# Performance work log

Measured on AMD Instinct MI355X. Metric: run time of the kernel, lower is better.

The kernel has to match this reference:

```python
import jax, jax.numpy as jnp
import numpy as np

B, S, DIN, DOUT, H = 4, 2048, 512, 512, 8
DH = DOUT // H
EPS = 1e-5


def _conv_bn(x, conv_w, conv_b, bn_gamma, bn_beta, bn_mean, bn_var):
    # x: [B, S, DIN] -> permute to [B, DIN, S] like torch
    xc = jnp.transpose(x, (0, 2, 1))
    y = jax.lax.conv_general_dilated(
        xc, conv_w, window_strides=(1,), padding=[(3, 3)],
        dimension_numbers=('NCH', 'OIH', 'NCH'))  # [B, DOUT, S]
    y = y + conv_b[None, :, None]
    # BatchNorm1d in eval mode: normalize per channel with running stats
    inv = jax.lax.rsqrt(bn_var + EPS)
    y = (y - bn_mean[None, :, None]) * (inv * bn_gamma)[None, :, None] + bn_beta[None, :, None]
    return jnp.transpose(y, (0, 2, 1))  # back to [B, S, DOUT]


def setup_inputs() -> dict:
    key = jax.random.key(0)
    ks = jax.random.split(key, 4)
    return {
        'q': jax.random.normal(ks[0], (B, S, DIN), dtype=jnp.float32),
        'k': jax.random.normal(ks[1], (B, S, DIN), dtype=jnp.float32),
        'v': jax.random.normal(ks[2], (B, S, DIN), dtype=jnp.float32),
        'conv_w': jax.random.normal(ks[3], (DOUT, DIN, 7), dtype=jnp.float32) * 0.02,
        'conv_b': jnp.zeros((DOUT,), jnp.float32),
        'bn_gamma': jnp.ones((DOUT,), jnp.float32),
        'bn_beta': jnp.zeros((DOUT,), jnp.float32),
        'bn_mean': jnp.zeros((DOUT,), jnp.float32),
        'bn_var': jnp.ones((DOUT,), jnp.float32),
        'ln_gamma': jnp.ones((DOUT,), jnp.float32),
        'ln_beta': jnp.zeros((DOUT,), jnp.float32),
    }


def reference(q, k, v, conv_w, conv_b, bn_gamma, bn_beta, bn_mean, bn_var,
              ln_gamma, ln_beta):
    # shared conv+BN preproc applied to q, k, v, then split into heads [B,S,H,DH]
    qh = _conv_bn(q, conv_w, conv_b, bn_gamma, bn_beta, bn_mean, bn_var).reshape(B, S, H, DH)
    kh = _conv_bn(k, conv_w, conv_b, bn_gamma, bn_beta, bn_mean, bn_var).reshape(B, S, H, DH)
    vh = _conv_bn(v, conv_w, conv_b, bn_gamma, bn_beta, bn_mean, bn_var).reshape(B, S, H, DH)
    # full QK^T score matrix, scaled, softmax, times V (mask is None)
    scores = jnp.einsum('bqhd,bkhd->bhqk', qh, kh) * (1.0 / np.sqrt(DH).astype(np.float32))
    probs = jax.nn.softmax(scores, axis=-1)
    out = jnp.einsum('bhqk,bkhd->bqhd', probs, vh).reshape(B, S, DOUT)
    # dropout(p=0) is identity; final LayerNorm over feature dim
    mu = jnp.mean(out, axis=-1, keepdims=True)
    var = jnp.mean(jnp.square(out - mu), axis=-1, keepdims=True)
    return (out - mu) * jax.lax.rsqrt(var + EPS) * ln_gamma + ln_beta
```

## Files before the change

kernel.cpp:

```cpp
#include <hip/hip_runtime.h>
#include <hip/hip_bf16.h>


#define B_ 4
#define S_ 2048
#define DIN_ 512
#define DOUT_ 512
#define H_ 8
#define DH_ 64
#define EPS_ 1e-5f
#define SP_ 2054

using bf16x8 = __attribute__((ext_vector_type(8))) short;
using f32x4  = __attribute__((ext_vector_type(4))) float;

__device__ __forceinline__ unsigned short f2bf(float x) {
    union { float f; unsigned u; } v; v.f = x;
    unsigned r = v.u + 0x7FFF + ((v.u >> 16) & 1);
    return (unsigned short)(r >> 16);
}

__device__ __forceinline__ unsigned cvt2(float lo, float hi) {
    unsigned r;
    asm("v_cvt_pk_bf16_f32 %0, %1, %2" : "=v"(r) : "v"(lo), "v"(hi));
    return r;
}

__device__ __forceinline__ float fexp2(float x) {
    float r;
    asm("v_exp_f32 %0, %1" : "=v"(r) : "v"(x));
    return r;
}

typedef __attribute__((address_space(1))) const unsigned int GU32;
typedef __attribute__((address_space(3))) unsigned int LU32;
__device__ __forceinline__ void gl_lds16(const void* g, void* l) {
    __builtin_amdgcn_global_load_lds((GU32*)g, (LU32*)l, 16, 0, 0);
}

__global__ void cast_x(const float* __restrict__ q, const float* __restrict__ k,
                       const float* __restrict__ v, unsigned short* __restrict__ xb) {
    int i = blockIdx.x * 256 + threadIdx.x;
    int row = i >> 6;
    int cin = (i & 63) * 8;
    int tb = row / SP_;
    int pr = row - tb * SP_;
    int tensor = tb >> 2;
    int b = tb & 3;
    unsigned short* dst = xb + (size_t)row * DIN_ + cin;
    if (pr < 3 || pr >= SP_ - 3) {
        *reinterpret_cast<uint4*>(dst) = make_uint4(0, 0, 0, 0);
    } else {
        const float* src = (tensor == 0 ? q : (tensor == 1 ? k : v)) +
                           ((size_t)b * S_ + (pr - 3)) * DIN_ + cin;
        float4 a0 = *reinterpret_cast<const float4*>(src);
        float4 a1 = *reinterpret_cast<const float4*>(src + 4);
        uint4 o;
        o.x = cvt2(a0.x, a0.y); o.y = cvt2(a0.z, a0.w);
        o.z = cvt2(a1.x, a1.y); o.w = cvt2(a1.z, a1.w);
        *reinterpret_cast<uint4*>(dst) = o;
    }
}

__global__ void prep_w(const float* __restrict__ w, const float* __restrict__ cb,
                       const float* __restrict__ gamma, const float* __restrict__ beta,
                       const float* __restrict__ mean, const float* __restrict__ var,
                       unsigned short* __restrict__ w_eff, float* __restrict__ b_eff) {
    int gid = blockIdx.x * blockDim.x + threadIdx.x;
    if (gid < DOUT_) {
        float sc = gamma[gid] * rsqrtf(var[gid] + EPS_);
        b_eff[gid] = (cb[gid] - mean[gid]) * sc + beta[gid];
    }
    int total = 7 * DOUT_ * DIN_;
    for (int i = gid; i < total; i += gridDim.x * blockDim.x) {
        int t = i / (DOUT_ * DIN_);
        int rem = i - t * (DOUT_ * DIN_);
        int co = rem >> 9;
        int ci = rem & 511;
        float sc = gamma[co] * rsqrtf(var[co] + EPS_);
        w_eff[i] = f2bf(w[(co * DIN_ + ci) * 7 + t] * sc);
    }
}

__global__ __launch_bounds__(256, 3) void conv_bn(
        const unsigned short* __restrict__ xb,
        const unsigned short* __restrict__ w_eff,
        const float* __restrict__ b_eff,
        unsigned short* __restrict__ out3) {
    __shared__ alignas(16) unsigned short As[2][192 * 32];
    __shared__ alignas(16) unsigned short Bs[3][128 * 32];

    int orig = blockIdx.x;
    int bid = (orig & 7) * 96 + (orig >> 3);
    int tensor = bid >> 8;
    int rem = bid & 255;
    int batch = rem >> 6;
    int stile = (rem >> 2) & 15;
    int cotile = rem & 3;
    int s0 = stile * 128;
    int co0 = cotile * 128;

    const unsigned short* xp = xb + (size_t)(tensor * 4 + batch) * SP_ * DIN_;
    unsigned short* out = out3 + (size_t)tensor * (B_ * S_ * DOUT_) +
                          (size_t)batch * S_ * DOUT_;

    const int tid = threadIdx.x;
    const int l = tid & 63;
    const int wv = tid >> 6;
    const int g = l >> 4;
    const int c16 = l & 15;
    const int wrow = (wv >> 1) * 64;
    const int wcol = (wv & 1) * 64;

    const int dr4 = l >> 2;
    const int sch = ((l & 3) ^ ((l >> 3) & 3)) << 3;

#define STAGE_A(cc, buf) do {                                                   \
        _Pragma("unroll")                                                       \
        for (int j = 0; j < 3; ++j) {                                           \
            int r0 = (wv * 3 + j) * 16;                                         \
            int rs = r0 + dr4; if (rs > 133) rs = 133;                          \
            gl_lds16(xp + (size_t)(s0 + rs) * DIN_ + (cc) * 32 + sch,           \
                     &As[buf][r0 * 32]);                                        \
        }                                                                       \
    } while (0)

#define STAGE_B(cc, t, buf) do {                                                \
        const unsigned short* wp = w_eff + (size_t)(t) * (DOUT_ * DIN_) +       \
                                   (cc) * 32;                                   \
        _Pragma("unroll")                                                       \
        for (int j = 0; j < 2; ++j) {                                           \
            int r0 = (wv * 2 + j) * 16;                                         \
            gl_lds16(wp + (size_t)(co0 + r0 + dr4) * DIN_ + sch,                \
                     &Bs[buf][r0 * 32]);                                        \
        }                                                                       \
    } while (0)

    f32x4 acc[4][4] = {};

    STAGE_A(0, 0);
    STAGE_B(0, 0, 0);
    int bcur = 0;

    for (int cc = 0; cc < 16; ++cc) {
        const int ca = cc & 1;
        for (int t = 0; t < 7; ++t) {
            int bnext = (bcur == 2) ? 0 : bcur + 1;
            if (t < 6) {
                STAGE_B(cc, t + 1, bnext);
                asm volatile("s_waitcnt vmcnt(2)" ::: "memory");
            } else if (cc < 15) {
                STAGE_B(cc + 1, 0, bnext);
                STAGE_A(cc + 1, ca ^ 1);
                asm volatile("s_waitcnt vmcnt(5)" ::: "memory");
            } else {
                asm volatile("s_waitcnt vmcnt(0)" ::: "memory");
            }
            __builtin_amdgcn_s_barrier();

            const unsigned short* Ab = &As[ca][0];
            const unsigned short* Bb = &Bs[bcur][0];
            bf16x8 af[4], bfv[4];
#pragma unroll
            for (int m = 0; m < 4; ++m) {
                int r = wrow + m * 16 + c16 + t;
                af[m] = *reinterpret_cast<const bf16x8*>(
                    &Ab[r * 32 + ((g ^ ((r >> 1) & 3)) << 3)]);
            }
#pragma unroll
            for (int n = 0; n < 4; ++n) {
                int rb = wcol + n * 16 + c16;
                bfv[n] = *reinterpret_cast<const bf16x8*>(
                    &Bb[rb * 32 + ((g ^ ((rb >> 1) & 3)) << 3)]);
            }
            __builtin_amdgcn_s_setprio(1);
#pragma unroll
            for (int m = 0; m < 4; ++m)
#pragma unroll
                for (int n = 0; n < 4; ++n)
                    acc[m][n] = __builtin_amdgcn_mfma_f32_16x16x32_bf16(
                        af[m], bfv[n], acc[m][n], 0, 0, 0);
            __builtin_amdgcn_s_setprio(0);
            bcur = bnext;
        }
    }

    float osc = (tensor == 0) ? 0.125f * 1.44269504f : 1.0f;
#pragma unroll
    for (int m = 0; m < 4; ++m) {
        int rowb = s0 + wrow + m * 16 + 4 * g;
#pragma unroll
        for (int n = 0; n < 4; ++n) {
            int col = co0 + wcol + n * 16 + c16;
            float be = b_eff[col];
#pragma unroll
            for (int ri = 0; ri < 4; ++ri)
                out[(size_t)(rowb + ri) * DOUT_ + col] =
                    f2bf((acc[m][n][ri] + be) * osc);
        }
    }
#undef STAGE_A
#undef STAGE_B
}

__global__ void transpose_v(const unsigned short* __restrict__ vh,
                            unsigned short* __restrict__ vt) {
    __shared__ alignas(16) unsigned short T[64 * 64];
    int bid = blockIdx.x;
    int stile = bid & 31;
    int bh = bid >> 5;
    int b = bh >> 3;
    int h = bh & 7;
    int s0 = stile * 64;
    const unsigned short* src = vh + ((size_t)b * S_ + s0) * DOUT_ + h * DH_;
    unsigned short* dst = vt + (size_t)bh * DH_ * S_ + s0;
    int tid = threadIdx.x;
#pragma unroll
    for (int it = 0; it < 2; ++it) {
        int idx = tid + it * 256;
        int s = idx >> 3, dhc = idx & 7;
        uint4 val = *reinterpret_cast<const uint4*>(&src[(size_t)s * DOUT_ + dhc * 8]);
        *reinterpret_cast<uint4*>(&T[s * 64 + ((dhc ^ (s & 7) ^ ((s >> 3) & 7)) << 3)]) = val;
    }
    __syncthreads();
#pragma unroll
    for (int it = 0; it < 2; ++it) {
        int idx = tid + it * 256;
        int dh = idx >> 3, sc = idx & 7;
        unsigned short tmp[8];
#pragma unroll
        for (int j = 0; j < 8; ++j) {
            int s = sc * 8 + j;
            tmp[j] = T[s * 64 + (((dh >> 3) ^ (s & 7) ^ ((s >> 3) & 7)) << 3) + (dh & 7)];
        }
        *reinterpret_cast<uint4*>(&dst[(size_t)dh * S_ + sc * 8]) =
            *reinterpret_cast<const uint4*>(tmp);
    }
}

__global__ __launch_bounds__(256, 4) void attn(const unsigned short* __restrict__ qh,
                     const unsigned short* __restrict__ kh,
                     const unsigned short* __restrict__ vt,
                     float* __restrict__ out) {
    __shared__ alignas(16) unsigned short Ks[2][64 * 64];
    __shared__ alignas(16) unsigned short Vs[2][64 * 64];

    const int tid = threadIdx.x;
    const int l = tid & 63;
    const int wv = tid >> 6;
    const int g = l >> 4;
    const int c16 = l & 15;

    const int bid = blockIdx.x;
    const int qt = bid & 31;
    const int bh = bid >> 5;
    const int b = bh >> 3;
    const int h = bh & 7;
    const int s0 = qt * 64;

    const unsigned short* qp = qh + (size_t)b * S_ * DOUT_ + h * DH_;
    const unsigned short* kp = kh + (size_t)b * S_ * DOUT_ + h * DH_;
    const unsigned short* vp = vt + (size_t)bh * DH_ * S_;

    bf16x8 qf[2];
    {
        int row = s0 + wv * 16 + c16;
        qf[0] = *reinterpret_cast<const bf16x8*>(&qp[(size_t)row * DOUT_ + 8 * g]);
        qf[1] = *reinterpret_cast<const bf16x8*>(&qp[(size_t)row * DOUT_ + 32 + 8 * g]);
    }

    const int l3 = l >> 3;
    const int kchunk8 = ((l & 7) ^ l3) * 8;

#define STAGE(kt, buf) do {                                                          \
        const unsigned short* kgp = kp + (size_t)(kt) * 64 * DOUT_;                  \
        const unsigned short* vgp = vp + (size_t)(kt) * 64;                          \
        _Pragma("unroll")                                                            \
        for (int i = 0; i < 2; ++i) {                                                \
            int K0 = wv * 16 + i * 8;                                                \
            gl_lds16(kgp + (size_t)(K0 + l3) * DOUT_ + kchunk8, &Ks[buf][K0 * 64]);  \
            gl_lds16(vgp + (size_t)(K0 + l3) * S_   + kchunk8, &Vs[buf][K0 * 64]);   \
        }                                                                            \
    } while (0)

    f32x4 oacc[4] = {};
    float mrow = -1e30f, lrow = 0.f;

    const int sA = ((l & 16) << 1) | c16;
    const int sB = sA + 16;
    const bool hi = (l & 32) != 0;

    STAGE(0, 0);

    const int NT = S_ / 64;
    for (int kt = 0; kt < NT; ++kt) {
        const int cur = kt & 1;
        if (kt + 1 < NT) {
            STAGE(kt + 1, 1 - cur);
            asm volatile("s_waitcnt vmcnt(4)" ::: "memory");
        } else {
            asm volatile("s_waitcnt vmcnt(0)" ::: "memory");
        }
        __builtin_amdgcn_s_barrier();

        const char* KsB = (const char*)&Ks[cur][0];
        f32x4 sf[4] = {};
#pragma unroll
        for (int kk = 0; kk < 2; ++kk) {
            bf16x8 kf[4];
#pragma unroll
            for (int n = 0; n < 4; ++n)
                kf[n] = *reinterpret_cast<const bf16x8*>(
                    KsB + (n * 16 + c16) * 128 + (((4 * kk + g) ^ (l & 7)) << 4));
            __builtin_amdgcn_s_setprio(1);
#pragma unroll
            for (int n = 0; n < 4; ++n)
                sf[n] = __builtin_amdgcn_mfma_f32_16x16x32_bf16(kf[n], qf[kk], sf[n], 0, 0, 0);
            __builtin_amdgcn_s_setprio(0);
        }

        float t0 = fmaxf(fmaxf(sf[0][0], sf[0][1]), fmaxf(sf[0][2], sf[0][3]));
        float t1 = fmaxf(fmaxf(sf[1][0], sf[1][1]), fmaxf(sf[1][2], sf[1][3]));
        float t2 = fmaxf(fmaxf(sf[2][0], sf[2][1]), fmaxf(sf[2][2], sf[2][3]));
        float t3 = fmaxf(fmaxf(sf[3][0], sf[3][1]), fmaxf(sf[3][2], sf[3][3]));
        float m0 = fmaxf(fmaxf(t0, t1), fmaxf(t2, t3));
        m0 = fmaxf(m0, __shfl_xor(m0, 16, 64));
        m0 = fmaxf(m0, __shfl_xor(m0, 32, 64));
        if (!__all(m0 <= mrow + 8.f)) {
            float mnew = fmaxf(mrow, m0);
            float corr = fexp2(mrow - mnew);
            mrow = mnew;
            lrow *= corr;
#pragma unroll
            for (int n = 0; n < 4; ++n) {
                oacc[n][0] *= corr; oacc[n][1] *= corr;
                oacc[n][2] *= corr; oacc[n][3] *= corr;
            }
        }
        unsigned pk[4][2];
        float rsn[4];
#pragma unroll
        for (int n = 0; n < 4; ++n) {
            float p0 = fexp2(sf[n][0] - mrow);
            float p1 = fexp2(sf[n][1] - mrow);
            float p2 = fexp2(sf[n][2] - mrow);
            float p3 = fexp2(sf[n][3] - mrow);
            rsn[n] = (p0 + p1) + (p2 + p3);
            pk[n][0] = cvt2(p0, p1);
            pk[n][1] = cvt2(p2, p3);
        }
        float rs = (rsn[0] + rsn[1]) + (rsn[2] + rsn[3]);
        rs += __shfl_xor(rs, 16, 64);
        rs += __shfl_xor(rs, 32, 64);
        lrow += rs;

        const char* VsB = (const char*)&Vs[cur][0];
#pragma unroll
        for (int kk = 0; kk < 2; ++kk) {
            unsigned a0 = __shfl((int)pk[2 * kk][0], sA, 64);
            unsigned a1 = __shfl((int)pk[2 * kk][1], sA, 64);
            unsigned a2 = __shfl((int)pk[2 * kk][0], sB, 64);
            unsigned a3 = __shfl((int)pk[2 * kk][1], sB, 64);
            unsigned b0 = __shfl((int)pk[2 * kk + 1][0], sA, 64);
            unsigned b1 = __shfl((int)pk[2 * kk + 1][1], sA, 64);
            unsigned b2 = __shfl((int)pk[2 * kk + 1][0], sB, 64);
            unsigned b3 = __shfl((int)pk[2 * kk + 1][1], sB, 64);
            union { unsigned w[4]; bf16x8 v; } pu;
            pu.w[0] = hi ? b0 : a0;
            pu.w[1] = hi ? b1 : a1;
            pu.w[2] = hi ? b2 : a2;
            pu.w[3] = hi ? b3 : a3;
            bf16x8 vfr[4];
#pragma unroll
            for (int n = 0; n < 4; ++n)
                vfr[n] = *reinterpret_cast<const bf16x8*>(
                    VsB + (n * 16 + c16) * 128 + (((4 * kk + g) ^ (l & 7)) << 4));
            __builtin_amdgcn_s_setprio(1);
#pragma unroll
            for (int n = 0; n < 4; ++n)
                oacc[n] = __builtin_amdgcn_mfma_f32_16x16x32_bf16(vfr[n], pu.v, oacc[n], 0, 0, 0);
            __builtin_amdgcn_s_setprio(0);
        }
        __builtin_amdgcn_s_barrier();
    }

    {
        int row = s0 + wv * 16 + c16;
        float inv = 1.0f / lrow;
        float* op = out + (size_t)b * S_ * DOUT_ + h * DH_ + (size_t)row * DOUT_;
#pragma unroll
        for (int n = 0; n < 4; ++n) {
            f32x4 o = oacc[n];
            o[0] *= inv; o[1] *= inv; o[2] *= inv; o[3] *= inv;
            *reinterpret_cast<f32x4*>(&op[n * 16 + 4 * g]) = o;
        }
    }
#undef STAGE
}

__global__ void lnorm(float* __restrict__ out, const float* __restrict__ gamma,
                      const float* __restrict__ beta) {
    int tid = threadIdx.x;
    int lane = tid & 63;
    int wv = tid >> 6;
    int row = blockIdx.x * 4 + wv;
    float* p = out + (size_t)row * DOUT_;
    float4 v0 = *reinterpret_cast<const float4*>(&p[lane * 8]);
    float4 v1 = *reinterpret_cast<const float4*>(&p[lane * 8 + 4]);
    float s = v0.x + v0.y + v0.z + v0.w + v1.x + v1.y + v1.z + v1.w;
    float sq = v0.x * v0.x + v0.y * v0.y + v0.z * v0.z + v0.w * v0.w +
               v1.x * v1.x + v1.y * v1.y + v1.z * v1.z + v1.w * v1.w;
    for (int off = 1; off < 64; off <<= 1) {
        s += __shfl_xor(s, off, 64);
        sq += __shfl_xor(sq, off, 64);
    }
    float mu = s * (1.0f / 512.0f);
    float var = sq * (1.0f / 512.0f) - mu * mu;
    float rstd = rsqrtf(fmaxf(var, 0.f) + EPS_);
    float4 g0 = *reinterpret_cast<const float4*>(&gamma[lane * 8]);
    float4 g1 = *reinterpret_cast<const float4*>(&gamma[lane * 8 + 4]);
    float4 b0 = *reinterpret_cast<const float4*>(&beta[lane * 8]);
    float4 b1 = *reinterpret_cast<const float4*>(&beta[lane * 8 + 4]);
    float4 o0, o1;
    o0.x = (v0.x - mu) * rstd * g0.x + b0.x;
    o0.y = (v0.y - mu) * rstd * g0.y + b0.y;
    o0.z = (v0.z - mu) * rstd * g0.z + b0.z;
    o0.w = (v0.w - mu) * rstd * g0.w + b0.w;
    o1.x = (v1.x - mu) * rstd * g1.x + b1.x;
    o1.y = (v1.y - mu) * rstd * g1.y + b1.y;
    o1.z = (v1.z - mu) * rstd * g1.z + b1.z;
    o1.w = (v1.w - mu) * rstd * g1.w + b1.w;
    *reinterpret_cast<float4*>(&p[lane * 8]) = o0;
    *reinterpret_cast<float4*>(&p[lane * 8 + 4]) = o1;
}

extern "C" void kernel_launch(void* const* d_in, const int* in_sizes, int n_in,
                              void* d_out, int out_size, void* d_ws, size_t ws_size,
                              hipStream_t stream) {
    const float* q        = (const float*)d_in[0];
    const float* k        = (const float*)d_in[1];
    const float* v        = (const float*)d_in[2];
    const float* conv_w   = (const float*)d_in[3];
    const float* conv_b   = (const float*)d_in[4];
    const float* bn_gamma = (const float*)d_in[5];
    const float* bn_beta  = (const float*)d_in[6];
    const float* bn_mean  = (const float*)d_in[7];
    const float* bn_var   = (const float*)d_in[8];
    const float* ln_gamma = (const float*)d_in[9];
    const float* ln_beta  = (const float*)d_in[10];

    unsigned short* qh    = (unsigned short*)d_ws;
    unsigned short* kh    = qh + (size_t)B_ * S_ * DOUT_;
    unsigned short* vh    = kh + (size_t)B_ * S_ * DOUT_;
    unsigned short* w_eff = vh + (size_t)B_ * S_ * DOUT_;
    float* b_eff          = (float*)(w_eff + (size_t)7 * DOUT_ * DIN_);
    unsigned short* xb    = (unsigned short*)(b_eff + DOUT_);
    unsigned short* vt    = xb;

    float* out = (float*)d_out;

    cast_x<<<dim3(6162), dim3(256), 0, stream>>>(q, k, v, xb);
    prep_w<<<dim3(7168), dim3(256), 0, stream>>>(conv_w, conv_b, bn_gamma, bn_beta,
                                                 bn_mean, bn_var, w_eff, b_eff);
    conv_bn<<<dim3(768), dim3(256), 0, stream>>>(xb, w_eff, b_eff, qh);
    transpose_v<<<dim3(1024), dim3(256), 0, stream>>>(vh, vt);
    attn<<<dim3(1024), dim3(256), 0, stream>>>(qh, kh, vt, out);
    lnorm<<<dim3(2048), dim3(256), 0, stream>>>(out, ln_gamma, ln_beta);
}
```

Before: 186.0 us.

## Split attention over key dimension and fuse partial combine into LayerNorm

The attention kernel now splits the 2048 keys into two halves, launching 2048 blocks that each write unnormalized bf16 partial outputs plus running max and sum. A new combine_ln kernel merges the two partials with the log-sum-exp rescaling and applies LayerNorm in the same pass, replacing the old lnorm. The point is to fill more of the GPU with work: 1024 blocks was small relative to the CU count, and launch bounds are raised to 5 waves. The costs are extra partial-output traffic, rounding the partials to bf16, and a larger workspace.

```diff
diff --git a/kernel.cpp b/kernel.cpp
--- a/kernel.cpp
+++ b/kernel.cpp
@@ -30,6 +30,11 @@
     float r;
     asm("v_exp_f32 %0, %1" : "=v"(r) : "v"(x));
     return r;
+}
+
+__device__ __forceinline__ float bf2f(unsigned short u) {
+    union { unsigned u; float f; } v; v.u = ((unsigned)u) << 16;
+    return v.f;
 }
 
 typedef __attribute__((address_space(1))) const unsigned int GU32;
@@ -238,10 +243,11 @@
     }
 }
 
-__global__ __launch_bounds__(256, 4) void attn(const unsigned short* __restrict__ qh,
+__global__ __launch_bounds__(256, 5) void attn(const unsigned short* __restrict__ qh,
                      const unsigned short* __restrict__ kh,
                      const unsigned short* __restrict__ vt,
-                     float* __restrict__ out) {
+                     unsigned short* __restrict__ part,
+                     float2* __restrict__ ml) {
     __shared__ alignas(16) unsigned short Ks[2][64 * 64];
     __shared__ alignas(16) unsigned short Vs[2][64 * 64];
 
@@ -252,8 +258,10 @@
     const int c16 = l & 15;
 
     const int bid = blockIdx.x;
-    const int qt = bid & 31;
-    const int bh = bid >> 5;
+    const int ks = bid >> 10;
+    const int r10 = bid & 1023;
+    const int qt = r10 & 31;
+    const int bh = r10 >> 5;
     const int b = bh >> 3;
     const int h = bh & 7;
     const int s0 = qt * 64;
@@ -290,13 +298,13 @@
     const int sB = sA + 16;
     const bool hi = (l & 32) != 0;
 
-    STAGE(0, 0);
-
-    const int NT = S_ / 64;
-    for (int kt = 0; kt < NT; ++kt) {
-        const int cur = kt & 1;
-        if (kt + 1 < NT) {
-            STAGE(kt + 1, 1 - cur);
+    const int t0 = ks * 16;
+    STAGE(t0, 0);
+
+    for (int i = 0; i < 16; ++i) {
+        const int cur = i & 1;
+        if (i + 1 < 16) {
+            STAGE(t0 + i + 1, 1 - cur);
             asm volatile("s_waitcnt vmcnt(4)" ::: "memory");
         } else {
             asm volatile("s_waitcnt vmcnt(0)" ::: "memory");
@@ -319,11 +327,11 @@
             __builtin_amdgcn_s_setprio(0);
         }
 
-        float t0 = fmaxf(fmaxf(sf[0][0], sf[0][1]), fmaxf(sf[0][2], sf[0][3]));
-        float t1 = fmaxf(fmaxf(sf[1][0], sf[1][1]), fmaxf(sf[1][2], sf[1][3]));
-        float t2 = fmaxf(fmaxf(sf[2][0], sf[2][1]), fmaxf(sf[2][2], sf[2][3]));
-        float t3 = fmaxf(fmaxf(sf[3][0], sf[3][1]), fmaxf(sf[3][2], sf[3][3]));
-        float m0 = fmaxf(fmaxf(t0, t1), fmaxf(t2, t3));
+        float u0 = fmaxf(fmaxf(sf[0][0], sf[0][1]), fmaxf(sf[0][2], sf[0][3]));
+        float u1 = fmaxf(fmaxf(sf[1][0], sf[1][1]), fmaxf(sf[1][2], sf[1][3]));
+        float u2 = fmaxf(fmaxf(sf[2][0], sf[2][1]), fmaxf(sf[2][2], sf[2][3]));
+        float u3 = fmaxf(fmaxf(sf[3][0], sf[3][1]), fmaxf(sf[3][2], sf[3][3]));
+        float m0 = fmaxf(fmaxf(u0, u1), fmaxf(u2, u3));
         m0 = fmaxf(m0, __shfl_xor(m0, 16, 64));
         m0 = fmaxf(m0, __shfl_xor(m0, 32, 64));
         if (!__all(m0 <= mrow + 8.f)) {
@@ -386,30 +394,57 @@
 
     {
         int row = s0 + wv * 16 + c16;
-        float inv = 1.0f / lrow;
-        float* op = out + (size_t)b * S_ * DOUT_ + h * DH_ + (size_t)row * DOUT_;
+        unsigned short* pp = part + (((size_t)ks * 32 + bh) * S_ + row) * DH_;
 #pragma unroll
         for (int n = 0; n < 4; ++n) {
-            f32x4 o = oacc[n];
-            o[0] *= inv; o[1] *= inv; o[2] *= inv; o[3] *= inv;
-            *reinterpret_cast<f32x4*>(&op[n * 16 + 4 * g]) = o;
-        }
+            uint2 w;
+            w.x = cvt2(oacc[n][0], oacc[n][1]);
+            w.y = cvt2(oacc[n][2], oacc[n][3]);
+            *reinterpret_cast<uint2*>(&pp[n * 16 + 4 * g]) = w;
+        }
+        if (g == 0)
+            ml[((size_t)ks * 32 + bh) * S_ + row] = make_float2(mrow, lrow);
     }
 #undef STAGE
 }
 
-__global__ void lnorm(float* __restrict__ out, const float* __restrict__ gamma,
-                      const float* __restrict__ beta) {
+__global__ void combine_ln(const unsigned short* __restrict__ part,
+                           const float2* __restrict__ ml,
+                           const float* __restrict__ gamma,
+                           const float* __restrict__ beta,
+                           float* __restrict__ out) {
     int tid = threadIdx.x;
     int lane = tid & 63;
     int wv = tid >> 6;
     int row = blockIdx.x * 4 + wv;
-    float* p = out + (size_t)row * DOUT_;
-    float4 v0 = *reinterpret_cast<const float4*>(&p[lane * 8]);
-    float4 v1 = *reinterpret_cast<const float4*>(&p[lane * 8 + 4]);
-    float s = v0.x + v0.y + v0.z + v0.w + v1.x + v1.y + v1.z + v1.w;
-    float sq = v0.x * v0.x + v0.y * v0.y + v0.z * v0.z + v0.w * v0.w +
-               v1.x * v1.x + v1.y * v1.y + v1.z * v1.z + v1.w * v1.w;
+    int b = row >> 11;
+    int q = row & 2047;
+    int h = lane >> 3;
+    int dh0 = (lane & 7) * 8;
+
+    size_t idx0 = ((size_t)(b * 8 + h)) * S_ + q;
+    size_t idx1 = ((size_t)32 + b * 8 + h) * S_ + q;
+    uint4 r0 = *reinterpret_cast<const uint4*>(&part[idx0 * DH_ + dh0]);
+    uint4 r1 = *reinterpret_cast<const uint4*>(&part[idx1 * DH_ + dh0]);
+    float2 ml0 = ml[idx0];
+    float2 ml1 = ml[idx1];
+
+    float m = fmaxf(ml0.x, ml1.x);
+    float w0 = fexp2(ml0.x - m);
+    float w1 = fexp2(ml1.x - m);
+    float linv = 1.0f / (w0 * ml0.y + w1 * ml1.y);
+
+    const unsigned short* e0 = reinterpret_cast<const unsigned short*>(&r0);
+    const unsigned short* e1 = reinterpret_cast<const unsigned short*>(&r1);
+    float o[8];
+    float s = 0.f, sq = 0.f;
+#pragma unroll
+    for (int j = 0; j < 8; ++j) {
+        float v = (w0 * bf2f(e0[j]) + w1 * bf2f(e1[j])) * linv;
+        o[j] = v;
+        s += v;
+        sq += v * v;
+    }
     for (int off = 1; off < 64; off <<= 1) {
         s += __shfl_xor(s, off, 64);
         sq += __shfl_xor(sq, off, 64);
@@ -417,21 +452,24 @@
     float mu = s * (1.0f / 512.0f);
     float var = sq * (1.0f / 512.0f) - mu * mu;
     float rstd = rsqrtf(fmaxf(var, 0.f) + EPS_);
-    float4 g0 = *reinterpret_cast<const float4*>(&gamma[lane * 8]);
-    float4 g1 = *reinterpret_cast<const float4*>(&gamma[lane * 8 + 4]);
-    float4 b0 = *reinterpret_cast<const float4*>(&beta[lane * 8]);
-    float4 b1 = *reinterpret_cast<const float4*>(&beta[lane * 8 + 4]);
+
+    int f0 = lane * 8;
+    float4 g0 = *reinterpret_cast<const float4*>(&gamma[f0]);
+    float4 g1 = *reinterpret_cast<const float4*>(&gamma[f0 + 4]);
+    float4 b0 = *reinterpret_cast<const float4*>(&beta[f0]);
+    float4 b1 = *reinterpret_cast<const float4*>(&beta[f0 + 4]);
     float4 o0, o1;
-    o0.x = (v0.x - mu) * rstd * g0.x + b0.x;
-    o0.y = (v0.y - mu) * rstd * g0.y + b0.y;
-    o0.z = (v0.z - mu) * rstd * g0.z + b0.z;
-    o0.w = (v0.w - mu) * rstd * g0.w + b0.w;
-    o1.x = (v1.x - mu) * rstd * g1.x + b1.x;
-    o1.y = (v1.y - mu) * rstd * g1.y + b1.y;
-    o1.z = (v1.z - mu) * rstd * g1.z + b1.z;
-    o1.w = (v1.w - mu) * rstd * g1.w + b1.w;
-    *reinterpret_cast<float4*>(&p[lane * 8]) = o0;
-    *reinterpret_cast<float4*>(&p[lane * 8 + 4]) = o1;
+    o0.x = (o[0] - mu) * rstd * g0.x + b0.x;
+    o0.y = (o[1] - mu) * rstd * g0.y + b0.y;
+    o0.z = (o[2] - mu) * rstd * g0.z + b0.z;
+    o0.w = (o[3] - mu) * rstd * g0.w + b0.w;
+    o1.x = (o[4] - mu) * rstd * g1.x + b1.x;
+    o1.y = (o[5] - mu) * rstd * g1.y + b1.y;
+    o1.z = (o[6] - mu) * rstd * g1.z + b1.z;
+    o1.w = (o[7] - mu) * rstd * g1.w + b1.w;
+    float* op = out + (size_t)row * DOUT_ + f0;
+    *reinterpret_cast<float4*>(op) = o0;
+    *reinterpret_cast<float4*>(op + 4) = o1;
 }
 
 extern "C" void kernel_launch(void* const* d_in, const int* in_sizes, int n_in,
@@ -456,6 +494,8 @@
     float* b_eff          = (float*)(w_eff + (size_t)7 * DOUT_ * DIN_);
     unsigned short* xb    = (unsigned short*)(b_eff + DOUT_);
     unsigned short* vt    = xb;
+    unsigned short* part  = xb + (size_t)12 * SP_ * DIN_;
+    float2* ml            = (float2*)(part + (size_t)2 * B_ * H_ * S_ * DH_);
 
     float* out = (float*)d_out;
 
@@ -464,6 +504,6 @@
                                                  bn_mean, bn_var, w_eff, b_eff);
     conv_bn<<<dim3(768), dim3(256), 0, stream>>>(xb, w_eff, b_eff, qh);
     transpose_v<<<dim3(1024), dim3(256), 0, stream>>>(vh, vt);
-    attn<<<dim3(1024), dim3(256), 0, stream>>>(qh, kh, vt, out);
-    lnorm<<<dim3(2048), dim3(256), 0, stream>>>(out, ln_gamma, ln_beta);
-}
+    attn<<<dim3(2048), dim3(256), 0, stream>>>(qh, kh, vt, part, ml);
+    combine_ln<<<dim3(2048), dim3(256), 0, stream>>>(part, ml, ln_gamma, ln_beta, out);
+}
```

Measured after the change: 185.3 us. Within noise of the previous version (-0.4%).
